# Performance work log

Measured on AMD Instinct MI355X. Metric: run time of the kernel, lower is better.

The kernel has to match this reference:

```python
import jax, jax.numpy as jnp
import numpy as np

B, P, NF = 4, 12000, 64
XS, YS = 512, 512


def setup_inputs() -> dict:
    key = jax.random.key(0)
    k1, k2, k3 = jax.random.split(key, 3)
    pillars = jax.random.normal(k1, (B, P, NF), dtype=jnp.float32)
    coord = jax.random.randint(k2, (B, P, 3), 0, XS)  # cols: (unused, y, x)
    contains_pillars = jax.random.randint(k3, (B, P), 0, 2)
    return {"pillars": pillars, "coord": coord,
            "contains_pillars": contains_pillars, "xsize": XS, "ysize": YS}


def reference(pillars, coord, contains_pillars, xsize, ysize):
    # Torch code gathers only pillars where contains_pillars==1 and scatter-adds
    # them per batch; masking the values to zero and scatter-adding everything
    # is mathematically identical (invalid entries contribute 0).
    batch, n_pillars, n_features = pillars.shape
    mask = (contains_pillars == 1).astype(pillars.dtype)        # [B, P]
    vals = pillars * mask[..., None]                            # [B, P, F]
    idx = coord[:, :, 1] * xsize + coord[:, :, 2]               # [B, P] flat grid index

    def scatter_one(v, i):
        # v: [P, F], i: [P] -> [xsize*ysize, F]
        return jnp.zeros((xsize * ysize, n_features), v.dtype).at[i].add(v)

    grid = jax.vmap(scatter_one)(vals, idx)                     # [B, XS*YS, F]
    return grid.reshape(batch, xsize, ysize, n_features).transpose(0, 3, 1, 2)
```

## Files before the change

### kernel.cpp

```cpp
#include <hip/hip_runtime.h>


#define NF 64
#define XS 512
#define YS 512
#define CELLS (XS * YS)
#define OVCAP 16384

__global__ void __launch_bounds__(256) build_slots(
    const int* __restrict__ coord,
    const int* __restrict__ contains,
    int* __restrict__ slot,
    int* __restrict__ overflow,
    int* __restrict__ counter,
    int BP, int P) {
  int gid = blockIdx.x * 256 + threadIdx.x;
  if (gid >= BP) return;
  if (contains[gid] == 0) return;
  int y = coord[gid * 3 + 1];
  int x = coord[gid * 3 + 2];
  int b = gid / P;
  int cell = (b << 18) + (y << 9) + x;
  int old = atomicExch(slot + cell, gid);
  if (old >= 0) {
    int k = atomicAdd(counter, 1);
    if (k < OVCAP) overflow[k] = old;
  }
}

__global__ void __launch_bounds__(256) fill_out(
    const float* __restrict__ pillars,
    const int* __restrict__ slot,
    float* __restrict__ out) {
  int by = blockIdx.x;
  int b = by >> 9;
  int y = by & 511;
  __shared__ int srow[XS];
  for (int i = threadIdx.x; i < XS; i += 256)
    srow[i] = slot[(b << 18) + (y << 9) + i];
  __syncthreads();
  int t = threadIdx.x;
  int x4 = (t & 127) << 2;
  int fbase = t >> 7;
  int s0 = srow[x4 + 0];
  int s1 = srow[x4 + 1];
  int s2 = srow[x4 + 2];
  int s3 = srow[x4 + 3];
  size_t rowoff = ((size_t)y << 9) + (size_t)x4;
#pragma unroll 4
  for (int fi = 0; fi < 32; ++fi) {
    int f = fi * 2 + fbase;
    float4 v;
    v.x = (s0 >= 0) ? pillars[((size_t)s0 << 6) + f] : 0.f;
    v.y = (s1 >= 0) ? pillars[((size_t)s1 << 6) + f] : 0.f;
    v.z = (s2 >= 0) ? pillars[((size_t)s2 << 6) + f] : 0.f;
    v.w = (s3 >= 0) ? pillars[((size_t)s3 << 6) + f] : 0.f;
    *(float4*)(out + (((size_t)(b * NF + f)) << 18) + rowoff) = v;
  }
}

__global__ void __launch_bounds__(256) fixup_overflow(
    const float* __restrict__ pillars,
    const int* __restrict__ coord,
    const int* __restrict__ overflow,
    const int* __restrict__ counter,
    float* __restrict__ out,
    int P) {
  int gid = blockIdx.x * 256 + threadIdx.x;
  int w = gid >> 6;
  int lane = gid & 63;
  int n = *counter;
  if (n > OVCAP) n = OVCAP;
  if (w >= n) return;
  int pg = overflow[w];
  int y = coord[pg * 3 + 1];
  int x = coord[pg * 3 + 2];
  int b = pg / P;
  atomicAdd(out + (((size_t)(b * NF + lane)) << 18) + ((size_t)y << 9) + x,
            pillars[((size_t)pg << 6) + lane]);
}

extern "C" void kernel_launch(void* const* d_in, const int* in_sizes, int n_in,
                              void* d_out, int out_size, void* d_ws, size_t ws_size,
                              hipStream_t stream) {
  const float* pillars  = (const float*)d_in[0];
  const int*   coord    = (const int*)d_in[1];
  const int*   contains = (const int*)d_in[2];
  float* out = (float*)d_out;

  const int BP = in_sizes[2];
  const int B  = out_size / (NF * CELLS);
  const int P  = BP / B;

  int* slot     = (int*)d_ws;
  int* counter  = (int*)((char*)d_ws + (size_t)B * CELLS * 4);
  int* overflow = counter + 4;

  hipMemsetAsync(slot, 0xFF, (size_t)B * CELLS * 4, stream);
  hipMemsetAsync(counter, 0, 4, stream);

  build_slots<<<(BP + 255) / 256, 256, 0, stream>>>(coord, contains, slot,
                                                    overflow, counter, BP, P);
  fill_out<<<B * YS, 256, 0, stream>>>(pillars, slot, out);
  fixup_overflow<<<(OVCAP * 64) / 256, 256, 0, stream>>>(pillars, coord, overflow,
                                                         counter, out, P);
}
```

Before: 296.3 us.

## Bin pillars per grid row and reduce duplicates in shared memory

Replaces the dense per-cell slot map, which needed a 4 MB memset, with per-row pillar lists built by atomic counters. Each fill block then loads its row's pillars into shared memory, merges duplicate x positions with LDS atomics, and writes the output with nontemporal stores. The overflow fixup now uses a small grid-stride launch. This drops the large memset and the scattered global gathers, at the cost of extra synchronisation and shared-memory use per block.

Result: no change. 292.0 us (-1.4%).

```diff
diff --git a/kernel.cpp b/kernel.cpp
--- a/kernel.cpp
+++ b/kernel.cpp
@@ -4,15 +4,18 @@
 #define NF 64
 #define XS 512
 #define YS 512
-#define CELLS (XS * YS)
+#define ROWCAP 64
 #define OVCAP 16384
 
-__global__ void __launch_bounds__(256) build_slots(
+typedef float vf4 __attribute__((ext_vector_type(4)));
+
+__global__ void __launch_bounds__(256) bin_pillars(
     const int* __restrict__ coord,
     const int* __restrict__ contains,
-    int* __restrict__ slot,
-    int* __restrict__ overflow,
-    int* __restrict__ counter,
+    int* __restrict__ rowcnt,
+    int* __restrict__ rowlist,
+    int* __restrict__ ovcnt,
+    int* __restrict__ ovlist,
     int BP, int P) {
   int gid = blockIdx.x * 256 + threadIdx.x;
   if (gid >= BP) return;
@@ -20,64 +23,96 @@
   int y = coord[gid * 3 + 1];
   int x = coord[gid * 3 + 2];
   int b = gid / P;
-  int cell = (b << 18) + (y << 9) + x;
-  int old = atomicExch(slot + cell, gid);
-  if (old >= 0) {
-    int k = atomicAdd(counter, 1);
-    if (k < OVCAP) overflow[k] = old;
+  int by = (b << 9) | y;
+  int k = atomicAdd(rowcnt + by, 1);
+  if (k < ROWCAP) {
+    rowlist[by * ROWCAP + k] = (x << 16) | gid;
+  } else {
+    int o = atomicAdd(ovcnt, 1);
+    if (o < OVCAP) ovlist[o] = gid;
   }
 }
 
 __global__ void __launch_bounds__(256) fill_out(
     const float* __restrict__ pillars,
-    const int* __restrict__ slot,
+    const int* __restrict__ rowcnt,
+    const int* __restrict__ rowlist,
     float* __restrict__ out) {
   int by = blockIdx.x;
   int b = by >> 9;
   int y = by & 511;
-  __shared__ int srow[XS];
-  for (int i = threadIdx.x; i < XS; i += 256)
-    srow[i] = slot[(b << 18) + (y << 9) + i];
+  __shared__ int xmap[XS];
+  __shared__ float prow[ROWCAP * 65];
+
+  int t = threadIdx.x;
+  xmap[t] = -1;
+  xmap[t + 256] = -1;
   __syncthreads();
-  int t = threadIdx.x;
+
+  int n = rowcnt[by];
+  if (n > ROWCAP) n = ROWCAP;
+
+  int myold = -1;
+  if (t < n) {
+    int e = rowlist[by * ROWCAP + t];
+    int x = e >> 16;
+    myold = atomicCAS(&xmap[x], -1, t);
+  }
+  __syncthreads();
+
+  int grp = t >> 6, lane = t & 63;
+  for (int k = grp; k < n; k += 4) {
+    int g = rowlist[by * ROWCAP + k] & 0xFFFF;
+    prow[k * 65 + lane] = pillars[((size_t)g << 6) + lane];
+  }
+  __syncthreads();
+
+  if (myold >= 0) {
+    for (int f = 0; f < NF; ++f)
+      atomicAdd(&prow[myold * 65 + f], prow[t * 65 + f]);
+  }
+  __syncthreads();
+
   int x4 = (t & 127) << 2;
   int fbase = t >> 7;
-  int s0 = srow[x4 + 0];
-  int s1 = srow[x4 + 1];
-  int s2 = srow[x4 + 2];
-  int s3 = srow[x4 + 3];
+  int s0 = xmap[x4 + 0];
+  int s1 = xmap[x4 + 1];
+  int s2 = xmap[x4 + 2];
+  int s3 = xmap[x4 + 3];
   size_t rowoff = ((size_t)y << 9) + (size_t)x4;
 #pragma unroll 4
   for (int fi = 0; fi < 32; ++fi) {
     int f = fi * 2 + fbase;
-    float4 v;
-    v.x = (s0 >= 0) ? pillars[((size_t)s0 << 6) + f] : 0.f;
-    v.y = (s1 >= 0) ? pillars[((size_t)s1 << 6) + f] : 0.f;
-    v.z = (s2 >= 0) ? pillars[((size_t)s2 << 6) + f] : 0.f;
-    v.w = (s3 >= 0) ? pillars[((size_t)s3 << 6) + f] : 0.f;
-    *(float4*)(out + (((size_t)(b * NF + f)) << 18) + rowoff) = v;
+    vf4 v;
+    v.x = (s0 >= 0) ? prow[s0 * 65 + f] : 0.f;
+    v.y = (s1 >= 0) ? prow[s1 * 65 + f] : 0.f;
+    v.z = (s2 >= 0) ? prow[s2 * 65 + f] : 0.f;
+    v.w = (s3 >= 0) ? prow[s3 * 65 + f] : 0.f;
+    __builtin_nontemporal_store(v, (vf4*)(out + (((size_t)(b * NF + f)) << 18) + rowoff));
   }
 }
 
 __global__ void __launch_bounds__(256) fixup_overflow(
     const float* __restrict__ pillars,
     const int* __restrict__ coord,
-    const int* __restrict__ overflow,
-    const int* __restrict__ counter,
+    const int* __restrict__ ovlist,
+    const int* __restrict__ ovcnt,
     float* __restrict__ out,
     int P) {
   int gid = blockIdx.x * 256 + threadIdx.x;
   int w = gid >> 6;
   int lane = gid & 63;
-  int n = *counter;
+  int n = *ovcnt;
   if (n > OVCAP) n = OVCAP;
-  if (w >= n) return;
-  int pg = overflow[w];
-  int y = coord[pg * 3 + 1];
-  int x = coord[pg * 3 + 2];
-  int b = pg / P;
-  atomicAdd(out + (((size_t)(b * NF + lane)) << 18) + ((size_t)y << 9) + x,
-            pillars[((size_t)pg << 6) + lane]);
+  int nw = gridDim.x * 4;
+  for (int i = w; i < n; i += nw) {
+    int g = ovlist[i];
+    int y = coord[g * 3 + 1];
+    int x = coord[g * 3 + 2];
+    int b = g / P;
+    atomicAdd(out + (((size_t)(b * NF + lane)) << 18) + ((size_t)y << 9) + x,
+              pillars[((size_t)g << 6) + lane]);
+  }
 }
 
 extern "C" void kernel_launch(void* const* d_in, const int* in_sizes, int n_in,
@@ -89,19 +124,19 @@
   float* out = (float*)d_out;
 
   const int BP = in_sizes[2];
-  const int B  = out_size / (NF * CELLS);
+  const int B  = out_size / (NF * XS * YS);
   const int P  = BP / B;
+  const int NROW = B * YS;
 
-  int* slot     = (int*)d_ws;
-  int* counter  = (int*)((char*)d_ws + (size_t)B * CELLS * 4);
-  int* overflow = counter + 4;
+  int* rowcnt  = (int*)d_ws;
+  int* ovcnt   = rowcnt + NROW;
+  int* rowlist = ovcnt + 4;
+  int* ovlist  = rowlist + NROW * ROWCAP;
 
-  hipMemsetAsync(slot, 0xFF, (size_t)B * CELLS * 4, stream);
-  hipMemsetAsync(counter, 0, 4, stream);
+  (void)hipMemsetAsync(rowcnt, 0, (size_t)(NROW + 4) * sizeof(int), stream);
 
-  build_slots<<<(BP + 255) / 256, 256, 0, stream>>>(coord, contains, slot,
-                                                    overflow, counter, BP, P);
-  fill_out<<<B * YS, 256, 0, stream>>>(pillars, slot, out);
-  fixup_overflow<<<(OVCAP * 64) / 256, 256, 0, stream>>>(pillars, coord, overflow,
-                                                         counter, out, P);
+  bin_pillars<<<(BP + 255) / 256, 256, 0, stream>>>(coord, contains, rowcnt,
+                                                    rowlist, ovcnt, ovlist, BP, P);
+  fill_out<<<NROW, 256, 0, stream>>>(pillars, rowcnt, rowlist, out);
+  fixup_overflow<<<64, 256, 0, stream>>>(pillars, coord, ovlist, ovcnt, out, P);
 }
```
